# Kernel optimization log

Hardware: AMD Instinct MI355X
Metric: run time of the kernel (lower is better)

The kernel has to match this reference:

```python
import jax, jax.numpy as jnp
import numpy as np

N_NODES = 50000
N_EDGES = 800000


def _gat_conv(x, src, dst, n, W, a_src, a_dst, b, concat):
    # x: [N, Fin]; W: [Fin, H*C]; a_src/a_dst: [H, C]; b: [H*C] or [C]
    H, C = a_src.shape
    h = (x @ W).reshape(n, H, C)                     # [N,H,C]
    alpha_src = jnp.sum(h * a_src[None], axis=-1)    # [N,H]
    alpha_dst = jnp.sum(h * a_dst[None], axis=-1)    # [N,H]
    e = alpha_src[src] + alpha_dst[dst]              # [E,H]
    e = jax.nn.leaky_relu(e, negative_slope=0.2)
    # segment softmax over incoming edges of each dst node
    m = jax.ops.segment_max(e, dst, num_segments=n)  # [N,H]
    ex = jnp.exp(e - m[dst])
    s = jax.ops.segment_sum(ex, dst, num_segments=n)
    alpha = ex / (s[dst] + 1e-16)                    # [E,H]
    msg = h[src] * alpha[:, :, None]                 # [E,H,C]
    out = jax.ops.segment_sum(msg, dst, num_segments=n)  # [N,H,C]
    out = out.reshape(n, H * C) if concat else out.mean(axis=1)
    return out + b


def setup_inputs() -> dict:
    key = jax.random.key(0)
    ks = jax.random.split(key, 12)
    d = {}
    d['x'] = jax.random.normal(ks[0], (N_NODES, 128), dtype=jnp.float32)
    d['edge_index'] = jax.random.randint(ks[1], (2, N_EDGES), 0, N_NODES, dtype=jnp.int32)
    s = 0.1
    d['w1'] = jax.random.normal(ks[2], (128, 128), dtype=jnp.float32) * s
    d['att_src1'] = jax.random.normal(ks[3], (2, 64), dtype=jnp.float32) * s
    d['att_dst1'] = jax.random.normal(ks[4], (2, 64), dtype=jnp.float32) * s
    d['b1'] = jnp.zeros((128,), jnp.float32)
    d['w2'] = jax.random.normal(ks[5], (128, 128), dtype=jnp.float32) * s
    d['att_src2'] = jax.random.normal(ks[6], (2, 64), dtype=jnp.float32) * s
    d['att_dst2'] = jax.random.normal(ks[7], (2, 64), dtype=jnp.float32) * s
    d['b2'] = jnp.zeros((128,), jnp.float32)
    d['w3'] = jax.random.normal(ks[8], (128, 40), dtype=jnp.float32) * s
    d['att_src3'] = jax.random.normal(ks[9], (1, 40), dtype=jnp.float32) * s
    d['att_dst3'] = jax.random.normal(ks[10], (1, 40), dtype=jnp.float32) * s
    d['b3'] = jnp.zeros((40,), jnp.float32)
    return d


def reference(x, edge_index, w1, att_src1, att_dst1, b1,
              w2, att_src2, att_dst2, b2, w3, att_src3, att_dst3, b3):
    n = x.shape[0]
    # PyG GATConv adds self-loops by default
    loop = jnp.arange(n, dtype=edge_index.dtype)
    src = jnp.concatenate([edge_index[0], loop])
    dst = jnp.concatenate([edge_index[1], loop])
    h = _gat_conv(x, src, dst, n, w1, att_src1, att_dst1, b1, concat=True)
    h = jax.nn.elu(h)  # dropout skipped (eval mode)
    h = _gat_conv(h, src, dst, n, w2, att_src2, att_dst2, b2, concat=True)
    h = jax.nn.elu(h)
    out = _gat_conv(h, src, dst, n, w3, att_src3, att_dst3, b3, concat=False)
    return out
```

## Files before the change

### kernel.cpp

```cpp
#include <hip/hip_runtime.h>
#include <hip/hip_fp16.h>

#define NN 50000
#define NE 800000
#define E2 850000
#define SCAN_NB 49

static inline int cdiv(long long a, int b) { return (int)((a + b - 1) / b); }

using half8  = __attribute__((ext_vector_type(8))) _Float16;
using floatx4 = __attribute__((ext_vector_type(4))) float;

struct __align__(16) h2x4 { __half2 a, b, c, d; };
struct __align__(8)  h2x2 { __half2 a, b; };

__device__ __forceinline__ void edge_sd(const int* __restrict__ ei, int e, int& s, int& d) {
    if (e < NE) { s = ei[e]; d = ei[NE + e]; }
    else { s = e - NE; d = s; }
}

__global__ __launch_bounds__(256) void cvt_f2h(const float* __restrict__ in,
                                               __half* __restrict__ out, int n4) {
    int i = blockIdx.x * 256 + threadIdx.x;
    if (i >= n4) return;
    float4 v = *(const float4*)&in[(size_t)i * 4];
    h2x2 st;
    st.a = __floats2half2_rn(v.x, v.y);
    st.b = __floats2half2_rn(v.z, v.w);
    *(h2x2*)&out[(size_t)i * 4] = st;
}

__global__ __launch_bounds__(256) void cvt_wT(const float* __restrict__ w,
                                              __half* __restrict__ wt, int M) {
    int i = blockIdx.x * 256 + threadIdx.x;
    if (i >= 128 * M) return;
    int k = i / M, n = i % M;
    wt[n * 128 + k] = __float2half(w[i]);
}

__global__ __launch_bounds__(256) void rank_pass(const int* __restrict__ ei,
                                                 int* __restrict__ deg,
                                                 int* __restrict__ rank) {
    int e = blockIdx.x * 256 + threadIdx.x;
    if (e >= E2) return;
    int d = (e < NE) ? ei[NE + e] : (e - NE);
    rank[e] = atomicAdd(&deg[d], 1);
}

__global__ __launch_bounds__(256) void scan1(const int* __restrict__ deg,
                                             int* __restrict__ loc,
                                             int* __restrict__ bsums) {
    __shared__ int wsum[4];
    int base = blockIdx.x * 1024 + threadIdx.x * 4;
    int4 v = make_int4(0, 0, 0, 0);
    if (base + 3 < NN) v = *(const int4*)&deg[base];
    else {
        if (base + 0 < NN) v.x = deg[base + 0];
        if (base + 1 < NN) v.y = deg[base + 1];
        if (base + 2 < NN) v.z = deg[base + 2];
    }
    v.y += v.x; v.z += v.y; v.w += v.z;
    int lane = threadIdx.x & 63;
    int wid = threadIdx.x >> 6;
    int t = v.w;
#pragma unroll
    for (int off = 1; off < 64; off <<= 1) {
        int u = __shfl_up(t, off, 64);
        if (lane >= off) t += u;
    }
    int excl = t - v.w;
    if (lane == 63) wsum[wid] = t;
    __syncthreads();
    int woff = 0;
    for (int w = 0; w < wid; ++w) woff += wsum[w];
    int add = excl + woff;
    int4 o = make_int4(v.x + add, v.y + add, v.z + add, v.w + add);
    if (base + 3 < NN) *(int4*)&loc[base] = o;
    else {
        if (base + 0 < NN) loc[base + 0] = o.x;
        if (base + 1 < NN) loc[base + 1] = o.y;
        if (base + 2 < NN) loc[base + 2] = o.z;
    }
    if (threadIdx.x == 255) bsums[blockIdx.x] = add + v.w;
}

__global__ __launch_bounds__(64) void scan2(int* __restrict__ bsums) {
    int lane = threadIdx.x;
    int orig = (lane < SCAN_NB) ? bsums[lane] : 0;
    int v = orig;
#pragma unroll
    for (int off = 1; off < 64; off <<= 1) {
        int u = __shfl_up(v, off, 64);
        if (lane >= off) v += u;
    }
    if (lane < SCAN_NB) bsums[lane] = v - orig;
}

__global__ __launch_bounds__(256) void scan3(const int* __restrict__ loc,
                                             const int* __restrict__ bsums,
                                             int* __restrict__ rowp) {
    int i = blockIdx.x * 256 + threadIdx.x;
    if (i == 0) rowp[0] = 0;
    if (i < NN) rowp[i + 1] = loc[i] + bsums[i >> 10];
}

__global__ __launch_bounds__(256) void csr_scatter2(const int* __restrict__ ei,
                                                    const int* __restrict__ rowp,
                                                    const int* __restrict__ rank,
                                                    int* __restrict__ csr_src) {
    int e = blockIdx.x * 256 + threadIdx.x;
    if (e >= E2) return;
    int s, d; edge_sd(ei, e, s, d);
    csr_src[rowp[d] + rank[e]] = s;
}

template<int MOUT, int H>
__global__ __launch_bounds__(256) void gemm16(const __half* __restrict__ X,
                                              const __half* __restrict__ WT,
                                              const float* __restrict__ aS,
                                              const float* __restrict__ aD,
                                              __half* __restrict__ Ho,
                                              float* __restrict__ osrc,
                                              float* __restrict__ odst) {
    constexpr int NT = (MOUT + 15) / 16;
    constexpr int NR = NT * 16;
    __shared__ __half wlds[NR * 136];
    const int tid = threadIdx.x;
    for (int i = tid * 8; i < MOUT * 128; i += 2048) {
        half8 v = *(const half8*)&WT[i];
        *(half8*)&wlds[(i >> 7) * 136 + (i & 127)] = v;
    }
    if (NR > MOUT) {
        for (int i = tid * 8; i < (NR - MOUT) * 128; i += 2048) {
            half8 z = {};
            *(half8*)&wlds[(MOUT + (i >> 7)) * 136 + (i & 127)] = z;
        }
    }
    __syncthreads();

    const int lane = tid & 63;
    const int wid = tid >> 6;
    const int r0 = blockIdx.x * 64 + wid * 16;
    const int arow = r0 + (lane & 15);
    const int lrow = (arow < NN) ? arow : (NN - 1);
    const int koff = (lane >> 4) * 8;
    const size_t xbase = (size_t)lrow * 128 + koff;
    half8 a0 = *(const half8*)&X[xbase];
    half8 a1 = *(const half8*)&X[xbase + 32];
    half8 a2 = *(const half8*)&X[xbase + 64];
    half8 a3 = *(const half8*)&X[xbase + 96];

    floatx4 acc[NT];
#pragma unroll
    for (int t = 0; t < NT; ++t) acc[t] = (floatx4){0.f, 0.f, 0.f, 0.f};

#pragma unroll
    for (int t = 0; t < NT; ++t) {
        const __half* wp = &wlds[(t * 16 + (lane & 15)) * 136 + koff];
        half8 b0 = *(const half8*)&wp[0];
        half8 b1 = *(const half8*)&wp[32];
        half8 b2 = *(const half8*)&wp[64];
        half8 b3 = *(const half8*)&wp[96];
        acc[t] = __builtin_amdgcn_mfma_f32_16x16x32_f16(a0, b0, acc[t], 0, 0, 0);
        acc[t] = __builtin_amdgcn_mfma_f32_16x16x32_f16(a1, b1, acc[t], 0, 0, 0);
        acc[t] = __builtin_amdgcn_mfma_f32_16x16x32_f16(a2, b2, acc[t], 0, 0, 0);
        acc[t] = __builtin_amdgcn_mfma_f32_16x16x32_f16(a3, b3, acc[t], 0, 0, 0);
    }

    const int cc = lane & 15;
    const int rbase = r0 + (lane >> 4) * 4;
    float ps[H][4], pd[H][4];
#pragma unroll
    for (int h = 0; h < H; ++h)
#pragma unroll
        for (int r = 0; r < 4; ++r) { ps[h][r] = 0.f; pd[h][r] = 0.f; }

#pragma unroll
    for (int t = 0; t < NT; ++t) {
        const int col = t * 16 + cc;
        const bool cv = (col < MOUT);
        const float as_ = cv ? aS[col] : 0.f;
        const float ad_ = cv ? aD[col] : 0.f;
        constexpr int hidx0 = 0;
        const int h = (H == 2) ? (t >> 2) : hidx0;
#pragma unroll
        for (int r = 0; r < 4; ++r) {
            ps[h][r] = fmaf(acc[t][r], as_, ps[h][r]);
            pd[h][r] = fmaf(acc[t][r], ad_, pd[h][r]);
            const int m = rbase + r;
            if (cv && m < NN) Ho[(size_t)m * MOUT + col] = __float2half(acc[t][r]);
        }
    }
#pragma unroll
    for (int off = 1; off <= 8; off <<= 1) {
#pragma unroll
        for (int h = 0; h < H; ++h)
#pragma unroll
            for (int r = 0; r < 4; ++r) {
                ps[h][r] += __shfl_xor(ps[h][r], off, 64);
                pd[h][r] += __shfl_xor(pd[h][r], off, 64);
            }
    }
    if (cc == 0) {
#pragma unroll
        for (int r = 0; r < 4; ++r) {
            const int m = rbase + r;
            if (m < NN) {
#pragma unroll
                for (int h = 0; h < H; ++h) {
                    osrc[m * H + h] = ps[h][r];
                    odst[m * H + h] = pd[h][r];
                }
            }
        }
    }
}

__global__ __launch_bounds__(256) void agg_h2(const int* __restrict__ rowp,
                                              const int* __restrict__ csr_src,
                                              const __half* __restrict__ Hf,
                                              const float* __restrict__ osrc,
                                              const float* __restrict__ odst,
                                              const float* __restrict__ bias,
                                              __half* __restrict__ outp) {
    int n = blockIdx.x * 4 + (threadIdx.x >> 6);
    if (n >= NN) return;
    int lane = threadIdx.x & 63;
    int i0 = rowp[n], i1 = rowp[n + 1];
    int c = lane & 15;
    int slot = lane >> 4;
    int c8 = c * 8;
    int h2 = c >> 3;
    float adh = odst[n * 2 + h2];
    bool pl = ((c & 7) == 0);

    float4 lo0{0.f,0.f,0.f,0.f}, hi0{0.f,0.f,0.f,0.f};
    float4 lo1{0.f,0.f,0.f,0.f}, hi1{0.f,0.f,0.f,0.f};
    float psum = 0.f;

    int idx = i0 + slot;
    for (; idx + 4 < i1; idx += 8) {
        int s0 = csr_src[idx];
        int s1 = csr_src[idx + 4];
        float e0 = osrc[s0 * 2 + h2] + adh;
        float e1 = osrc[s1 * 2 + h2] + adh;
        e0 = (e0 >= 0.f) ? e0 : 0.2f * e0;
        e1 = (e1 >= 0.f) ? e1 : 0.2f * e1;
        float p0 = __expf(e0);
        float p1 = __expf(e1);
        h2x4 hv0 = *(const h2x4*)&Hf[(size_t)s0 * 128 + c8];
        h2x4 hv1 = *(const h2x4*)&Hf[(size_t)s1 * 128 + c8];
        if (pl) psum += p0 + p1;
        float2 f;
        f = __half22float2(hv0.a); lo0.x = fmaf(f.x, p0, lo0.x); lo0.y = fmaf(f.y, p0, lo0.y);
        f = __half22float2(hv0.b); lo0.z = fmaf(f.x, p0, lo0.z); lo0.w = fmaf(f.y, p0, lo0.w);
        f = __half22float2(hv0.c); hi0.x = fmaf(f.x, p0, hi0.x); hi0.y = fmaf(f.y, p0, hi0.y);
        f = __half22float2(hv0.d); hi0.z = fmaf(f.x, p0, hi0.z); hi0.w = fmaf(f.y, p0, hi0.w);
        f = __half22float2(hv1.a); lo1.x = fmaf(f.x, p1, lo1.x); lo1.y = fmaf(f.y, p1, lo1.y);
        f = __half22float2(hv1.b); lo1.z = fmaf(f.x, p1, lo1.z); lo1.w = fmaf(f.y, p1, lo1.w);
        f = __half22float2(hv1.c); hi1.x = fmaf(f.x, p1, hi1.x); hi1.y = fmaf(f.y, p1, hi1.y);
        f = __half22float2(hv1.d); hi1.z = fmaf(f.x, p1, hi1.z); hi1.w = fmaf(f.y, p1, hi1.w);
    }
    if (idx < i1) {
        int s0 = csr_src[idx];
        float e0 = osrc[s0 * 2 + h2] + adh;
        e0 = (e0 >= 0.f) ? e0 : 0.2f * e0;
        float p0 = __expf(e0);
        h2x4 hv0 = *(const h2x4*)&Hf[(size_t)s0 * 128 + c8];
        if (pl) psum += p0;
        float2 f;
        f = __half22float2(hv0.a); lo0.x = fmaf(f.x, p0, lo0.x); lo0.y = fmaf(f.y, p0, lo0.y);
        f = __half22float2(hv0.b); lo0.z = fmaf(f.x, p0, lo0.z); lo0.w = fmaf(f.y, p0, lo0.w);
        f = __half22float2(hv0.c); hi0.x = fmaf(f.x, p0, hi0.x); hi0.y = fmaf(f.y, p0, hi0.y);
        f = __half22float2(hv0.d); hi0.z = fmaf(f.x, p0, hi0.z); hi0.w = fmaf(f.y, p0, hi0.w);
    }
    float4 lo{lo0.x + lo1.x, lo0.y + lo1.y, lo0.z + lo1.z, lo0.w + lo1.w};
    float4 hi{hi0.x + hi1.x, hi0.y + hi1.y, hi0.z + hi1.z, hi0.w + hi1.w};
#pragma unroll
    for (int off = 16; off <= 32; off <<= 1) {
        lo.x += __shfl_xor(lo.x, off, 64); lo.y += __shfl_xor(lo.y, off, 64);
        lo.z += __shfl_xor(lo.z, off, 64); lo.w += __shfl_xor(lo.w, off, 64);
        hi.x += __shfl_xor(hi.x, off, 64); hi.y += __shfl_xor(hi.y, off, 64);
        hi.z += __shfl_xor(hi.z, off, 64); hi.w += __shfl_xor(hi.w, off, 64);
        psum += __shfl_xor(psum, off, 64);
    }
    float sh = __shfl(psum, h2 * 8, 64);
    float inv = 1.f / (sh + 1e-16f);
    if (lane < 16) {
        float4 bl = *(const float4*)&bias[c8];
        float4 bh = *(const float4*)&bias[c8 + 4];
        float o0 = fmaf(lo.x, inv, bl.x), o1 = fmaf(lo.y, inv, bl.y);
        float o2 = fmaf(lo.z, inv, bl.z), o3 = fmaf(lo.w, inv, bl.w);
        float o4 = fmaf(hi.x, inv, bh.x), o5 = fmaf(hi.y, inv, bh.y);
        float o6 = fmaf(hi.z, inv, bh.z), o7 = fmaf(hi.w, inv, bh.w);
        o0 = (o0 > 0.f) ? o0 : (__expf(o0) - 1.f);
        o1 = (o1 > 0.f) ? o1 : (__expf(o1) - 1.f);
        o2 = (o2 > 0.f) ? o2 : (__expf(o2) - 1.f);
        o3 = (o3 > 0.f) ? o3 : (__expf(o3) - 1.f);
        o4 = (o4 > 0.f) ? o4 : (__expf(o4) - 1.f);
        o5 = (o5 > 0.f) ? o5 : (__expf(o5) - 1.f);
        o6 = (o6 > 0.f) ? o6 : (__expf(o6) - 1.f);
        o7 = (o7 > 0.f) ? o7 : (__expf(o7) - 1.f);
        h2x4 st;
        st.a = __floats2half2_rn(o0, o1);
        st.b = __floats2half2_rn(o2, o3);
        st.c = __floats2half2_rn(o4, o5);
        st.d = __floats2half2_rn(o6, o7);
        *(h2x4*)&outp[(size_t)n * 128 + c8] = st;
    }
}

__global__ __launch_bounds__(256) void agg_h1(const int* __restrict__ rowp,
                                              const int* __restrict__ csr_src,
                                              const __half* __restrict__ Hf,
                                              const float* __restrict__ osrc,
                                              const float* __restrict__ odst,
                                              const float* __restrict__ bias,
                                              float* __restrict__ outp) {
    int n = blockIdx.x * 4 + (threadIdx.x >> 6);
    if (n >= NN) return;
    int lane = threadIdx.x & 63;
    int i0 = rowp[n], i1 = rowp[n + 1];
    float ad = odst[n];
    int c = lane & 15;
    int slot = lane >> 4;
    bool cl = (c < 10);
    bool pl = (c == 0);
    float4 acc0{0.f,0.f,0.f,0.f}, acc1{0.f,0.f,0.f,0.f};
    float psum = 0.f;

    int idx = i0 + slot;
    for (; idx + 4 < i1; idx += 8) {
        int s0 = csr_src[idx];
        int s1 = csr_src[idx + 4];
        float e0 = osrc[s0] + ad;
        float e1 = osrc[s1] + ad;
        e0 = (e0 >= 0.f) ? e0 : 0.2f * e0;
        e1 = (e1 >= 0.f) ? e1 : 0.2f * e1;
        float p0 = __expf(e0);
        float p1 = __expf(e1);
        if (pl) psum += p0 + p1;
        if (cl) {
            h2x2 hv0 = *(const h2x2*)&Hf[(size_t)s0 * 40 + c * 4];
            h2x2 hv1 = *(const h2x2*)&Hf[(size_t)s1 * 40 + c * 4];
            float2 f;
            f = __half22float2(hv0.a); acc0.x = fmaf(f.x, p0, acc0.x); acc0.y = fmaf(f.y, p0, acc0.y);
            f = __half22float2(hv0.b); acc0.z = fmaf(f.x, p0, acc0.z); acc0.w = fmaf(f.y, p0, acc0.w);
            f = __half22float2(hv1.a); acc1.x = fmaf(f.x, p1, acc1.x); acc1.y = fmaf(f.y, p1, acc1.y);
            f = __half22float2(hv1.b); acc1.z = fmaf(f.x, p1, acc1.z); acc1.w = fmaf(f.y, p1, acc1.w);
        }
    }
    if (idx < i1) {
        int s0 = csr_src[idx];
        float e0 = osrc[s0] + ad;
        e0 = (e0 >= 0.f) ? e0 : 0.2f * e0;
        float p0 = __expf(e0);
        if (pl) psum += p0;
        if (cl) {
            h2x2 hv0 = *(const h2x2*)&Hf[(size_t)s0 * 40 + c * 4];
            float2 f;
            f = __half22float2(hv0.a); acc0.x = fmaf(f.x, p0, acc0.x); acc0.y = fmaf(f.y, p0, acc0.y);
            f = __half22float2(hv0.b); acc0.z = fmaf(f.x, p0, acc0.z); acc0.w = fmaf(f.y, p0, acc0.w);
        }
    }
    float4 acc{acc0.x + acc1.x, acc0.y + acc1.y, acc0.z + acc1.z, acc0.w + acc1.w};
#pragma unroll
    for (int off = 16; off <= 32; off <<= 1) {
        acc.x += __shfl_xor(acc.x, off, 64);
        acc.y += __shfl_xor(acc.y, off, 64);
        acc.z += __shfl_xor(acc.z, off, 64);
        acc.w += __shfl_xor(acc.w, off, 64);
        psum += __shfl_xor(psum, off, 64);
    }
    float sh = __shfl(psum, 0, 64);
    float inv = 1.f / (sh + 1e-16f);
    if (lane < 10) {
        float4 b = *(const float4*)&bias[lane * 4];
        float4 o;
        o.x = fmaf(acc.x, inv, b.x);
        o.y = fmaf(acc.y, inv, b.y);
        o.z = fmaf(acc.z, inv, b.z);
        o.w = fmaf(acc.w, inv, b.w);
        *(float4*)&outp[(size_t)n * 40 + lane * 4] = o;
    }
}

extern "C" void kernel_launch(void* const* d_in, const int* in_sizes, int n_in,
                              void* d_out, int out_size, void* d_ws, size_t ws_size,
                              hipStream_t stream) {
    const float* x   = (const float*)d_in[0];
    const int*   ei  = (const int*)d_in[1];
    const float* w1  = (const float*)d_in[2];
    const float* as1 = (const float*)d_in[3];
    const float* ad1 = (const float*)d_in[4];
    const float* b1  = (const float*)d_in[5];
    const float* w2  = (const float*)d_in[6];
    const float* as2 = (const float*)d_in[7];
    const float* ad2 = (const float*)d_in[8];
    const float* b2  = (const float*)d_in[9];
    const float* w3  = (const float*)d_in[10];
    const float* as3 = (const float*)d_in[11];
    const float* ad3 = (const float*)d_in[12];
    const float* b3  = (const float*)d_in[13];
    float* out = (float*)d_out;

    char* p = (char*)d_ws;
    __half* x16   = (__half*)p; p += (size_t)NN * 128 * 2;
    __half* h16   = (__half*)p; p += (size_t)NN * 128 * 2;
    __half* f16   = (__half*)p; p += (size_t)NN * 128 * 2;
    __half* wt1   = (__half*)p; p += (size_t)128 * 128 * 2;
    __half* wt2   = (__half*)p; p += (size_t)128 * 128 * 2;
    __half* wt3   = (__half*)p; p += (size_t)64 * 128 * 2;
    float*  osrc  = (float*)p;  p += (size_t)NN * 2 * 4;
    float*  odst  = (float*)p;  p += (size_t)NN * 2 * 4;
    int*    rowp  = (int*)p;    p += (size_t)(NN + 1) * 4;
    int*    deg   = (int*)p;    p += (size_t)NN * 4;
    int*    rank  = (int*)p;    p += (size_t)E2 * 4;
    int*    loc   = (int*)p;    p += (size_t)NN * 4;
    int*    bsums = (int*)p;    p += (size_t)64 * 4;
    int*    csrsrc= (int*)p;    p += (size_t)E2 * 4;

    const int edgeGrid = cdiv(E2, 256);
    const int nodeGrid = cdiv(NN, 4);
    const int gemmGrid = cdiv(NN, 64);

    hipMemsetAsync(deg, 0, (size_t)NN * 4, stream);
    rank_pass<<<edgeGrid, 256, 0, stream>>>(ei, deg, rank);
    scan1<<<SCAN_NB, 256, 0, stream>>>(deg, loc, bsums);
    scan2<<<1, 64, 0, stream>>>(bsums);
    scan3<<<cdiv(NN, 256), 256, 0, stream>>>(loc, bsums, rowp);
    csr_scatter2<<<edgeGrid, 256, 0, stream>>>(ei, rowp, rank, csrsrc);

    cvt_f2h<<<cdiv((long long)NN * 32, 256), 256, 0, stream>>>(x, x16, NN * 32);
    cvt_wT<<<cdiv(128 * 128, 256), 256, 0, stream>>>(w1, wt1, 128);
    cvt_wT<<<cdiv(128 * 128, 256), 256, 0, stream>>>(w2, wt2, 128);
    cvt_wT<<<cdiv(128 * 40, 256), 256, 0, stream>>>(w3, wt3, 40);

    gemm16<128, 2><<<gemmGrid, 256, 0, stream>>>(x16, wt1, as1, ad1, h16, osrc, odst);
    agg_h2<<<nodeGrid, 256, 0, stream>>>(rowp, csrsrc, h16, osrc, odst, b1, f16);

    gemm16<128, 2><<<gemmGrid, 256, 0, stream>>>(f16, wt2, as2, ad2, h16, osrc, odst);
    agg_h2<<<nodeGrid, 256, 0, stream>>>(rowp, csrsrc, h16, osrc, odst, b2, f16);

    gemm16<40, 1><<<gemmGrid, 256, 0, stream>>>(f16, wt3, as3, ad3, h16, osrc, odst);
    agg_h1<<<nodeGrid, 256, 0, stream>>>(rowp, csrsrc, h16, osrc, odst, b3, out);
}
```

Measured before the change: 214.9 us.

## Fuse prep kernels, merge scans, co-launch CSR scatter with GEMM, unroll aggregation

Replaces the memset and four conversion kernels with a single grid-stride prep kernel, and merges scan2 and scan3 into one kernel. The CSR scatter now runs as extra blocks of the first GEMM launch, which reduces launch count and lets the two overlap. The 128-wide GEMM output is staged through LDS so rows are written with coalesced 16-byte stores. The aggregation loops are unrolled to four edges per iteration for more memory-level parallelism. The cost is higher register pressure in the aggregation kernels and a GEMM kernel whose blocks do unequal work.

```diff
diff --git a/kernel.cpp b/kernel.cpp
--- a/kernel.cpp
+++ b/kernel.cpp
@@ -5,6 +5,7 @@
 #define NE 800000
 #define E2 850000
 #define SCAN_NB 49
+#define GEMM_BLKS 782
 
 static inline int cdiv(long long a, int b) { return (int)((a + b - 1) / b); }
 
@@ -19,23 +20,27 @@
     else { s = e - NE; d = s; }
 }
 
-__global__ __launch_bounds__(256) void cvt_f2h(const float* __restrict__ in,
-                                               __half* __restrict__ out, int n4) {
-    int i = blockIdx.x * 256 + threadIdx.x;
-    if (i >= n4) return;
-    float4 v = *(const float4*)&in[(size_t)i * 4];
-    h2x2 st;
-    st.a = __floats2half2_rn(v.x, v.y);
-    st.b = __floats2half2_rn(v.z, v.w);
-    *(h2x2*)&out[(size_t)i * 4] = st;
-}
-
-__global__ __launch_bounds__(256) void cvt_wT(const float* __restrict__ w,
-                                              __half* __restrict__ wt, int M) {
-    int i = blockIdx.x * 256 + threadIdx.x;
-    if (i >= 128 * M) return;
-    int k = i / M, n = i % M;
-    wt[n * 128 + k] = __float2half(w[i]);
+__global__ __launch_bounds__(256) void prep(const float* __restrict__ x, __half* __restrict__ x16,
+                                            const float* __restrict__ w1, __half* __restrict__ wt1,
+                                            const float* __restrict__ w2, __half* __restrict__ wt2,
+                                            const float* __restrict__ w3, __half* __restrict__ wt3,
+                                            int* __restrict__ deg) {
+    int tid = blockIdx.x * 256 + threadIdx.x;
+    int stride = gridDim.x * 256;
+    for (int i = tid; i < NN * 32; i += stride) {
+        float4 v = *(const float4*)&x[(size_t)i * 4];
+        h2x2 st;
+        st.a = __floats2half2_rn(v.x, v.y);
+        st.b = __floats2half2_rn(v.z, v.w);
+        *(h2x2*)&x16[(size_t)i * 4] = st;
+    }
+    for (int i = tid; i < 128 * 128; i += stride)
+        wt1[i] = __float2half(w1[(i & 127) * 128 + (i >> 7)]);
+    for (int i = tid; i < 128 * 128; i += stride)
+        wt2[i] = __float2half(w2[(i & 127) * 128 + (i >> 7)]);
+    for (int i = tid; i < 40 * 128; i += stride)
+        wt3[i] = __float2half(w3[(i & 127) * 40 + (i >> 7)]);
+    for (int i = tid; i < NN; i += stride) deg[i] = 0;
 }
 
 __global__ __launch_bounds__(256) void rank_pass(const int* __restrict__ ei,
@@ -84,47 +89,38 @@
     if (threadIdx.x == 255) bsums[blockIdx.x] = add + v.w;
 }
 
-__global__ __launch_bounds__(64) void scan2(int* __restrict__ bsums) {
-    int lane = threadIdx.x;
-    int orig = (lane < SCAN_NB) ? bsums[lane] : 0;
-    int v = orig;
-#pragma unroll
-    for (int off = 1; off < 64; off <<= 1) {
-        int u = __shfl_up(v, off, 64);
-        if (lane >= off) v += u;
-    }
-    if (lane < SCAN_NB) bsums[lane] = v - orig;
-}
-
-__global__ __launch_bounds__(256) void scan3(const int* __restrict__ loc,
-                                             const int* __restrict__ bsums,
-                                             int* __restrict__ rowp) {
-    int i = blockIdx.x * 256 + threadIdx.x;
+__global__ __launch_bounds__(256) void scan23(const int* __restrict__ loc,
+                                              const int* __restrict__ bsums,
+                                              int* __restrict__ rowp) {
+    __shared__ int sh_b[64];
+    int tid = threadIdx.x;
+    if (tid < 64) {
+        int orig = (tid < SCAN_NB) ? bsums[tid] : 0;
+        int v = orig;
+#pragma unroll
+        for (int off = 1; off < 64; off <<= 1) {
+            int u = __shfl_up(v, off, 64);
+            if (tid >= off) v += u;
+        }
+        sh_b[tid] = v - orig;
+    }
+    __syncthreads();
+    int i = blockIdx.x * 256 + tid;
     if (i == 0) rowp[0] = 0;
-    if (i < NN) rowp[i + 1] = loc[i] + bsums[i >> 10];
-}
-
-__global__ __launch_bounds__(256) void csr_scatter2(const int* __restrict__ ei,
-                                                    const int* __restrict__ rowp,
-                                                    const int* __restrict__ rank,
-                                                    int* __restrict__ csr_src) {
-    int e = blockIdx.x * 256 + threadIdx.x;
-    if (e >= E2) return;
-    int s, d; edge_sd(ei, e, s, d);
-    csr_src[rowp[d] + rank[e]] = s;
+    if (i < NN) rowp[i + 1] = loc[i] + sh_b[i >> 10];
 }
 
 template<int MOUT, int H>
-__global__ __launch_bounds__(256) void gemm16(const __half* __restrict__ X,
-                                              const __half* __restrict__ WT,
-                                              const float* __restrict__ aS,
-                                              const float* __restrict__ aD,
-                                              __half* __restrict__ Ho,
-                                              float* __restrict__ osrc,
-                                              float* __restrict__ odst) {
+__device__ __forceinline__ void gemm_body(int bid, const __half* __restrict__ X,
+                                          const __half* __restrict__ WT,
+                                          const float* __restrict__ aS,
+                                          const float* __restrict__ aD,
+                                          __half* __restrict__ Ho,
+                                          float* __restrict__ osrc,
+                                          float* __restrict__ odst,
+                                          __half* wlds) {
     constexpr int NT = (MOUT + 15) / 16;
     constexpr int NR = NT * 16;
-    __shared__ __half wlds[NR * 136];
     const int tid = threadIdx.x;
     for (int i = tid * 8; i < MOUT * 128; i += 2048) {
         half8 v = *(const half8*)&WT[i];
@@ -140,7 +136,7 @@
 
     const int lane = tid & 63;
     const int wid = tid >> 6;
-    const int r0 = blockIdx.x * 64 + wid * 16;
+    const int r0 = bid * 64 + wid * 16;
     const int arow = r0 + (lane & 15);
     const int lrow = (arow < NN) ? arow : (NN - 1);
     const int koff = (lane >> 4) * 8;
@@ -181,16 +177,45 @@
         const bool cv = (col < MOUT);
         const float as_ = cv ? aS[col] : 0.f;
         const float ad_ = cv ? aD[col] : 0.f;
-        constexpr int hidx0 = 0;
-        const int h = (H == 2) ? (t >> 2) : hidx0;
+        const int h = (H == 2) ? (t >> 2) : 0;
 #pragma unroll
         for (int r = 0; r < 4; ++r) {
             ps[h][r] = fmaf(acc[t][r], as_, ps[h][r]);
             pd[h][r] = fmaf(acc[t][r], ad_, pd[h][r]);
-            const int m = rbase + r;
-            if (cv && m < NN) Ho[(size_t)m * MOUT + col] = __float2half(acc[t][r]);
-        }
-    }
+        }
+    }
+
+    if constexpr (MOUT == 128) {
+        __syncthreads();
+        const int rowbase = wid * 16;
+#pragma unroll
+        for (int t = 0; t < NT; ++t)
+#pragma unroll
+            for (int r = 0; r < 4; ++r)
+                wlds[(rowbase + (lane >> 4) * 4 + r) * 136 + t * 16 + cc] =
+                    __float2half(acc[t][r]);
+        __syncthreads();
+#pragma unroll
+        for (int p2 = 0; p2 < 4; ++p2) {
+            int f = (p2 * 64 + lane) * 8;
+            int row = f >> 7, col = f & 127;
+            h2x4 v = *(h2x4*)&wlds[(rowbase + row) * 136 + col];
+            int grow = r0 + row;
+            if (grow < NN) *(h2x4*)&Ho[(size_t)grow * 128 + col] = v;
+        }
+    } else {
+#pragma unroll
+        for (int t = 0; t < NT; ++t) {
+            const int col = t * 16 + cc;
+            const bool cv = (col < MOUT);
+#pragma unroll
+            for (int r = 0; r < 4; ++r) {
+                const int m = rbase + r;
+                if (cv && m < NN) Ho[(size_t)m * MOUT + col] = __float2half(acc[t][r]);
+            }
+        }
+    }
+
 #pragma unroll
     for (int off = 1; off <= 8; off <<= 1) {
 #pragma unroll
@@ -214,6 +239,50 @@
             }
         }
     }
+}
+
+__global__ __launch_bounds__(256) void gemm16_k128(const __half* __restrict__ X,
+                                                   const __half* __restrict__ WT,
+                                                   const float* __restrict__ aS,
+                                                   const float* __restrict__ aD,
+                                                   __half* __restrict__ Ho,
+                                                   float* __restrict__ osrc,
+                                                   float* __restrict__ odst) {
+    __shared__ __half wlds[128 * 136];
+    gemm_body<128, 2>(blockIdx.x, X, WT, aS, aD, Ho, osrc, odst, wlds);
+}
+
+__global__ __launch_bounds__(256) void gemm16_k40(const __half* __restrict__ X,
+                                                  const __half* __restrict__ WT,
+                                                  const float* __restrict__ aS,
+                                                  const float* __restrict__ aD,
+                                                  __half* __restrict__ Ho,
+                                                  float* __restrict__ osrc,
+                                                  float* __restrict__ odst) {
+    __shared__ __half wlds[48 * 136];
+    gemm_body<40, 1>(blockIdx.x, X, WT, aS, aD, Ho, osrc, odst, wlds);
+}
+
+__global__ __launch_bounds__(256) void gemm1_scat(const __half* __restrict__ X,
+                                                  const __half* __restrict__ WT,
+                                                  const float* __restrict__ aS,
+                                                  const float* __restrict__ aD,
+                                                  __half* __restrict__ Ho,
+                                                  float* __restrict__ osrc,
+                                                  float* __restrict__ odst,
+                                                  const int* __restrict__ ei,
+                                                  const int* __restrict__ rowp,
+                                                  const int* __restrict__ rank,
+                                                  int* __restrict__ csr_src) {
+    __shared__ __half wlds[128 * 136];
+    if (blockIdx.x < GEMM_BLKS) {
+        gemm_body<128, 2>(blockIdx.x, X, WT, aS, aD, Ho, osrc, odst, wlds);
+        return;
+    }
+    int e = (blockIdx.x - GEMM_BLKS) * 256 + threadIdx.x;
+    if (e >= E2) return;
+    int s, d; edge_sd(ei, e, s, d);
+    csr_src[rowp[d] + rank[e]] = s;
 }
 
 __global__ __launch_bounds__(256) void agg_h2(const int* __restrict__ rowp,
@@ -239,29 +308,44 @@
     float psum = 0.f;
 
     int idx = i0 + slot;
-    for (; idx + 4 < i1; idx += 8) {
+    for (; idx + 12 < i1; idx += 16) {
         int s0 = csr_src[idx];
         int s1 = csr_src[idx + 4];
+        int s2 = csr_src[idx + 8];
+        int s3 = csr_src[idx + 12];
         float e0 = osrc[s0 * 2 + h2] + adh;
         float e1 = osrc[s1 * 2 + h2] + adh;
+        float e2 = osrc[s2 * 2 + h2] + adh;
+        float e3 = osrc[s3 * 2 + h2] + adh;
         e0 = (e0 >= 0.f) ? e0 : 0.2f * e0;
         e1 = (e1 >= 0.f) ? e1 : 0.2f * e1;
-        float p0 = __expf(e0);
-        float p1 = __expf(e1);
+        e2 = (e2 >= 0.f) ? e2 : 0.2f * e2;
+        e3 = (e3 >= 0.f) ? e3 : 0.2f * e3;
+        float p0 = __expf(e0), p1 = __expf(e1), p2 = __expf(e2), p3 = __expf(e3);
         h2x4 hv0 = *(const h2x4*)&Hf[(size_t)s0 * 128 + c8];
         h2x4 hv1 = *(const h2x4*)&Hf[(size_t)s1 * 128 + c8];
-        if (pl) psum += p0 + p1;
+        h2x4 hv2 = *(const h2x4*)&Hf[(size_t)s2 * 128 + c8];
+        h2x4 hv3 = *(const h2x4*)&Hf[(size_t)s3 * 128 + c8];
+        if (pl) psum += (p0 + p1) + (p2 + p3);
         float2 f;
         f = __half22float2(hv0.a); lo0.x = fmaf(f.x, p0, lo0.x); lo0.y = fmaf(f.y, p0, lo0.y);
         f = __half22float2(hv0.b); lo0.z = fmaf(f.x, p0, lo0.z); lo0.w = fmaf(f.y, p0, lo0.w);
         f = __half22float2(hv0.c); hi0.x = fmaf(f.x, p0, hi0.x); hi0.y = fmaf(f.y, p0, hi0.y);
         f = __half22float2(hv0.d); hi0.z = fmaf(f.x, p0, hi0.z); hi0.w = fmaf(f.y, p0, hi0.w);
-        f = __half22float2(hv1.a); lo1.x = fmaf(f.x, p1, lo1.x); lo1.y = fmaf(f.y, p1, lo1.y);
-        f = __half22float2(hv1.b); lo1.z = fmaf(f.x, p1, lo1.z); lo1.w = fmaf(f.y, p1, lo1.w);
-        f = __half22float2(hv1.c); hi1.x = fmaf(f.x, p1, hi1.x); hi1.y = fmaf(f.y, p1, hi1.y);
-        f = __half22float2(hv1.d); hi1.z = fmaf(f.x, p1, hi1.z); hi1.w = fmaf(f.y, p1, hi1.w);
-    }
-    if (idx < i1) {
+        f = __half22float2(hv1.a); lo0.x = fmaf(f.x, p1, lo0.x); lo0.y = fmaf(f.y, p1, lo0.y);
+        f = __half22float2(hv1.b); lo0.z = fmaf(f.x, p1, lo0.z); lo0.w = fmaf(f.y, p1, lo0.w);
+        f = __half22float2(hv1.c); hi0.x = fmaf(f.x, p1, hi0.x); hi0.y = fmaf(f.y, p1, hi0.y);
+        f = __half22float2(hv1.d); hi0.z = fmaf(f.x, p1, hi0.z); hi0.w = fmaf(f.y, p1, hi0.w);
+        f = __half22float2(hv2.a); lo1.x = fmaf(f.x, p2, lo1.x); lo1.y = fmaf(f.y, p2, lo1.y);
+        f = __half22float2(hv2.b); lo1.z = fmaf(f.x, p2, lo1.z); lo1.w = fmaf(f.y, p2, lo1.w);
+        f = __half22float2(hv2.c); hi1.x = fmaf(f.x, p2, hi1.x); hi1.y = fmaf(f.y, p2, hi1.y);
+        f = __half22float2(hv2.d); hi1.z = fmaf(f.x, p2, hi1.z); hi1.w = fmaf(f.y, p2, hi1.w);
+        f = __half22float2(hv3.a); lo1.x = fmaf(f.x, p3, lo1.x); lo1.y = fmaf(f.y, p3, lo1.y);
+        f = __half22float2(hv3.b); lo1.z = fmaf(f.x, p3, lo1.z); lo1.w = fmaf(f.y, p3, lo1.w);
+        f = __half22float2(hv3.c); hi1.x = fmaf(f.x, p3, hi1.x); hi1.y = fmaf(f.y, p3, hi1.y);
+        f = __half22float2(hv3.d); hi1.z = fmaf(f.x, p3, hi1.z); hi1.w = fmaf(f.y, p3, hi1.w);
+    }
+    for (; idx < i1; idx += 4) {
         int s0 = csr_src[idx];
         float e0 = osrc[s0 * 2 + h2] + adh;
         e0 = (e0 >= 0.f) ? e0 : 0.2f * e0;
@@ -330,27 +414,36 @@
     float psum = 0.f;
 
     int idx = i0 + slot;
-    for (; idx + 4 < i1; idx += 8) {
+    for (; idx + 12 < i1; idx += 16) {
         int s0 = csr_src[idx];
         int s1 = csr_src[idx + 4];
-        float e0 = osrc[s0] + ad;
-        float e1 = osrc[s1] + ad;
+        int s2 = csr_src[idx + 8];
+        int s3 = csr_src[idx + 12];
+        float e0 = osrc[s0] + ad, e1 = osrc[s1] + ad;
+        float e2 = osrc[s2] + ad, e3 = osrc[s3] + ad;
         e0 = (e0 >= 0.f) ? e0 : 0.2f * e0;
         e1 = (e1 >= 0.f) ? e1 : 0.2f * e1;
-        float p0 = __expf(e0);
-        float p1 = __expf(e1);
-        if (pl) psum += p0 + p1;
+        e2 = (e2 >= 0.f) ? e2 : 0.2f * e2;
+        e3 = (e3 >= 0.f) ? e3 : 0.2f * e3;
+        float p0 = __expf(e0), p1 = __expf(e1), p2 = __expf(e2), p3 = __expf(e3);
+        if (pl) psum += (p0 + p1) + (p2 + p3);
         if (cl) {
             h2x2 hv0 = *(const h2x2*)&Hf[(size_t)s0 * 40 + c * 4];
             h2x2 hv1 = *(const h2x2*)&Hf[(size_t)s1 * 40 + c * 4];
+            h2x2 hv2 = *(const h2x2*)&Hf[(size_t)s2 * 40 + c * 4];
+            h2x2 hv3 = *(const h2x2*)&Hf[(size_t)s3 * 40 + c * 4];
             float2 f;
             f = __half22float2(hv0.a); acc0.x = fmaf(f.x, p0, acc0.x); acc0.y = fmaf(f.y, p0, acc0.y);
             f = __half22float2(hv0.b); acc0.z = fmaf(f.x, p0, acc0.z); acc0.w = fmaf(f.y, p0, acc0.w);
             f = __half22float2(hv1.a); acc1.x = fmaf(f.x, p1, acc1.x); acc1.y = fmaf(f.y, p1, acc1.y);
             f = __half22float2(hv1.b); acc1.z = fmaf(f.x, p1, acc1.z); acc1.w = fmaf(f.y, p1, acc1.w);
-        }
-    }
-    if (idx < i1) {
+            f = __half22float2(hv2.a); acc0.x = fmaf(f.x, p2, acc0.x); acc0.y = fmaf(f.y, p2, acc0.y);
+            f = __half22float2(hv2.b); acc0.z = fmaf(f.x, p2, acc0.z); acc0.w = fmaf(f.y, p2, acc0.w);
+            f = __half22float2(hv3.a); acc1.x = fmaf(f.x, p3, acc1.x); acc1.y = fmaf(f.y, p3, acc1.y);
+            f = __half22float2(hv3.b); acc1.z = fmaf(f.x, p3, acc1.z); acc1.w = fmaf(f.y, p3, acc1.w);
+        }
+    }
+    for (; idx < i1; idx += 4) {
         int s0 = csr_src[idx];
         float e0 = osrc[s0] + ad;
         e0 = (e0 >= 0.f) ? e0 : 0.2f * e0;
@@ -422,26 +515,19 @@
 
     const int edgeGrid = cdiv(E2, 256);
     const int nodeGrid = cdiv(NN, 4);
-    const int gemmGrid = cdiv(NN, 64);
-
-    hipMemsetAsync(deg, 0, (size_t)NN * 4, stream);
+
+    prep<<<2048, 256, 0, stream>>>(x, x16, w1, wt1, w2, wt2, w3, wt3, deg);
     rank_pass<<<edgeGrid, 256, 0, stream>>>(ei, deg, rank);
     scan1<<<SCAN_NB, 256, 0, stream>>>(deg, loc, bsums);
-    scan2<<<1, 64, 0, stream>>>(bsums);
-    scan3<<<cdiv(NN, 256), 256, 0, stream>>>(loc, bsums, rowp);
-    csr_scatter2<<<edgeGrid, 256, 0, stream>>>(ei, rowp, rank, csrsrc);
-
-    cvt_f2h<<<cdiv((long long)NN * 32, 256), 256, 0, stream>>>(x, x16, NN * 32);
-    cvt_wT<<<cdiv(128 * 128, 256), 256, 0, stream>>>(w1, wt1, 128);
-    cvt_wT<<<cdiv(128 * 128, 256), 256, 0, stream>>>(w2, wt2, 128);
-    cvt_wT<<<cdiv(128 * 40, 256), 256, 0, stream>>>(w3, wt3, 40);
-
-    gemm16<128, 2><<<gemmGrid, 256, 0, stream>>>(x16, wt1, as1, ad1, h16, osrc, odst);
+    scan23<<<cdiv(NN, 256), 256, 0, stream>>>(loc, bsums, rowp);
+
+    gemm1_scat<<<GEMM_BLKS + edgeGrid, 256, 0, stream>>>(x16, wt1, as1, ad1, h16,
+                                                         osrc, odst, ei, rowp, rank, csrsrc);
     agg_h2<<<nodeGrid, 256, 0, stream>>>(rowp, csrsrc, h16, osrc, odst, b1, f16);
 
-    gemm16<128, 2><<<gemmGrid, 256, 0, stream>>>(f16, wt2, as2, ad2, h16, osrc, odst);
+    gemm16_k128<<<GEMM_BLKS, 256, 0, stream>>>(f16, wt2, as2, ad2, h16, osrc, odst);
     agg_h2<<<nodeGrid, 256, 0, stream>>>(rowp, csrsrc, h16, osrc, odst, b2, f16);
 
-    gemm16<40, 1><<<gemmGrid, 256, 0, stream>>>(f16, wt3, as3, ad3, h16, osrc, odst);
+    gemm16_k40<<<GEMM_BLKS, 256, 0, stream>>>(f16, wt3, as3, ad3, h16, osrc, odst);
     agg_h1<<<nodeGrid, 256, 0, stream>>>(rowp, csrsrc, h16, osrc, odst, b3, out);
 }
```

Result: faster. 198.8 us (-7.5%).
